# Optimization experiments

Measured on AMD Instinct MI355X. Metric: run time of the kernel, lower is better.

## Reference

```python
import jax, jax.numpy as jnp
import numpy as np

EPS = 1e-5


def _in_relu(y):
    # instance norm (no affine, biased var, eps=1e-5) + ReLU, y: [B,C,H,W]
    mu = jnp.mean(y, axis=(-2, -1), keepdims=True)
    var = jnp.mean((y - mu) ** 2, axis=(-2, -1), keepdims=True)
    return jax.nn.relu((y - mu) * jax.lax.rsqrt(var + EPS))


def _conv3(x, w, b):
    # x: [C,H,W], w: [O,I,3,3] -> [O,H,W]
    y = jax.lax.conv_general_dilated(x[None], w, (1, 1), ((1, 1), (1, 1)),
                                     dimension_numbers=('NCHW', 'OIHW', 'NCHW'))[0]
    return y + b[:, None, None]


def _mod_block(x, W, b, mod):
    # per-sample weight modulation: mod[n] * W, then conv+IN+relu; x: [B,C,H,W], mod: [B,O,I,3,3]
    y = jax.vmap(lambda xi, mi: _conv3(xi, mi * W, b))(x, mod)
    return _in_relu(y)


def _maxpool2(x):
    return jax.lax.reduce_window(x, -jnp.inf, jax.lax.max, (1, 1, 2, 2), (1, 1, 2, 2), 'VALID')


def _up2(x):
    B, C, H, W = x.shape
    # bilinear, half-pixel centers == PyTorch align_corners=False
    return jax.image.resize(x, (B, C, 2 * H, 2 * W), method='bilinear')


def _conv1x1(x, w, b):
    y = jax.lax.conv_general_dilated(x, w, (1, 1), 'VALID',
                                     dimension_numbers=('NCHW', 'OIHW', 'NCHW'))
    return y + b[None, :, None, None]


def setup_inputs() -> dict:
    key = jax.random.key(0)
    B, H, W = 8, 256, 256
    ks = iter(jax.random.split(key, 64))
    d = {}
    d['us_query_input'] = jax.random.normal(next(ks), (B, 1, H, W), jnp.float32)
    d['ksp_query_imgs'] = jax.random.normal(next(ks), (B, H, W, 2), jnp.float32)
    d['ksp_mask_query'] = jax.random.uniform(next(ks), (B, H, W), jnp.float32)
    down_io = [(1, 32), (32, 64), (64, 128), (128, 256)]
    up_io = [(512, 128), (256, 64), (128, 32), (64, 32)]
    for i, (ci, co) in enumerate(down_io):
        d[f'down_mod_{i}'] = jax.random.normal(next(ks), (B, co, ci, 3, 3), jnp.float32)
        d[f'W_d{i}'] = 0.05 * jax.random.normal(next(ks), (co, ci, 3, 3), jnp.float32)
        d[f'b_d{i}'] = 0.05 * jax.random.normal(next(ks), (co,), jnp.float32)
    d['latent_mod'] = jax.random.normal(next(ks), (B, 256, 256, 3, 3), jnp.float32)
    d['W_lat'] = 0.05 * jax.random.normal(next(ks), (256, 256, 3, 3), jnp.float32)
    d['b_lat'] = 0.05 * jax.random.normal(next(ks), (256,), jnp.float32)
    for i, (ci, co) in enumerate(up_io):
        d[f'up_mod_{i}'] = jax.random.normal(next(ks), (B, co, ci, 3, 3), jnp.float32)
        d[f'W_u{i}'] = 0.05 * jax.random.normal(next(ks), (co, ci, 3, 3), jnp.float32)
        d[f'b_u{i}'] = 0.05 * jax.random.normal(next(ks), (co,), jnp.float32)
    d['w_c1'] = 0.05 * jax.random.normal(next(ks), (16, 32, 1, 1), jnp.float32)
    d['b_c1'] = 0.05 * jax.random.normal(next(ks), (16,), jnp.float32)
    d['w_c2'] = 0.05 * jax.random.normal(next(ks), (1, 16, 1, 1), jnp.float32)
    d['b_c2'] = 0.05 * jax.random.normal(next(ks), (1,), jnp.float32)
    d['w_c3'] = 0.05 * jax.random.normal(next(ks), (1, 1, 1, 1), jnp.float32)
    d['b_c3'] = 0.05 * jax.random.normal(next(ks), (1,), jnp.float32)
    return d


def reference(us_query_input, ksp_query_imgs, ksp_mask_query,
              down_mod_0, down_mod_1, down_mod_2, down_mod_3,
              latent_mod, up_mod_0, up_mod_1, up_mod_2, up_mod_3,
              W_d0, b_d0, W_d1, b_d1, W_d2, b_d2, W_d3, b_d3,
              W_lat, b_lat,
              W_u0, b_u0, W_u1, b_u1, W_u2, b_u2, W_u3, b_u3,
              w_c1, b_c1, w_c2, b_c2, w_c3, b_c3):
    x0 = us_query_input
    out = x0
    skips = []
    downs = [(W_d0, b_d0, down_mod_0), (W_d1, b_d1, down_mod_1),
             (W_d2, b_d2, down_mod_2), (W_d3, b_d3, down_mod_3)]
    for Wc, bc, m in downs:
        out = _mod_block(out, Wc, bc, m)
        skips.append(out)
        out = _maxpool2(out)
    out = _mod_block(out, W_lat, b_lat, latent_mod)
    ups = [(W_u0, b_u0, up_mod_0), (W_u1, b_u1, up_mod_1),
           (W_u2, b_u2, up_mod_2), (W_u3, b_u3, up_mod_3)]
    for Wc, bc, m in ups:
        out = _up2(out)
        out = jnp.concatenate([out, skips.pop()], axis=1)
        out = _mod_block(out, Wc, bc, m)
    out = _conv1x1(_conv1x1(_conv1x1(out, w_c1, b_c1), w_c2, b_c2), w_c3, b_c3)
    out = out + x0
    # FFT data consistency
    pred = out[:, 0]                                  # [B,H,W]
    kpred = jnp.fft.fft2(pred, norm='ortho')
    ksp = ksp_query_imgs[..., 0] + 1j * ksp_query_imgs[..., 1]
    upd = ksp_mask_query * ksp + (1.0 - ksp_mask_query) * kpred
    img = jnp.fft.ifft2(upd, norm='ortho')
    return jnp.real(img)[:, None].astype(jnp.float32)   # [B,1,H,W]
```

## Files before the change

kernel.cpp:

```cpp
#include <hip/hip_runtime.h>


#define EPS_IN 1e-5f

typedef __attribute__((ext_vector_type(8))) short short8;
typedef __attribute__((ext_vector_type(4))) short short4_t;
typedef __attribute__((ext_vector_type(4))) float f32x4;

__device__ __forceinline__ short f2bf(float f) {
    unsigned u = __float_as_uint(f);
    unsigned r = (u + 0x7fffu + ((u >> 16) & 1u)) >> 16;
    return (short)r;
}
__device__ __forceinline__ float bf2f(short s) {
    return __uint_as_float(((unsigned)(unsigned short)s) << 16);
}

__global__ void zero_f(float* __restrict__ p, int n)
{
    int i = blockIdx.x * 256 + threadIdx.x;
    if (i < n) p[i] = 0.f;
}

__global__ void make_wm(const float* __restrict__ W, const float* __restrict__ mod,
                        short* __restrict__ wm, int Co, int Ci)
{
    int idx = blockIdx.x * 256 + threadIdx.x;
    int total = 8 * Co * Ci;
    if (idx >= total) return;
    int ci = idx % Ci;
    int rem = idx / Ci;
    int co = rem % Co;
    int b = rem / Co;
    const float* wp = W + (size_t)(co * Ci + ci) * 9;
    const float* mp = mod + ((size_t)((size_t)b * Co + co) * Ci + ci) * 9;
#pragma unroll
    for (int k = 0; k < 9; ++k)
        wm[(((size_t)(b * 9 + k) * Co + co) * Ci + ci)] = f2bf(wp[k] * mp[k]);
}

template <int VR, int NCOG>
__global__ __launch_bounds__(256) void conv3x3_cl(
    const short* __restrict__ x1, int Ci1,
    const short* __restrict__ x2,
    const short* __restrict__ wm,
    short* __restrict__ y,
    float2* __restrict__ stats,
    int Ci, int Co, int H, int W)
{
    constexpr int TH = 4 * VR, SH = TH + 2, SW = 18;
    __shared__ short s_x[SH][SW][32];
    __shared__ float s_red[4][4][NCOG][4][2];

    const int tid = threadIdx.x;
    const int lane = tid & 63, wv = tid >> 6;
    const int m = lane & 15, g = lane >> 4;
    const int tilesx = W >> 4;
    const int tx0 = (blockIdx.x % tilesx) * 16;
    const int ty0 = (blockIdx.x / tilesx) * TH;
    const int co0 = blockIdx.y * (16 * NCOG);
    const int b = blockIdx.z;
    const int Ci2 = Ci - Ci1;

    f32x4 acc[NCOG][VR];
#pragma unroll
    for (int cg = 0; cg < NCOG; ++cg)
#pragma unroll
        for (int r = 0; r < VR; ++r) acc[cg][r] = (f32x4)0.f;

    const short* wmb = wm + (size_t)b * 9 * Co * Ci;

    for (int ci0 = 0; ci0 < Ci; ci0 += 32) {
        const short* src; int C, cb;
        if (ci0 < Ci1) { src = x1 + (size_t)b * H * W * Ci1; C = Ci1; cb = ci0; }
        else           { src = x2 + (size_t)b * H * W * Ci2; C = Ci2; cb = ci0 - Ci1; }
        __syncthreads();
        for (int idx = tid; idx < SH * SW * 4; idx += 256) {
            int gg = idx & 3, pos = idx >> 2;
            int yy = pos / SW, xx = pos - yy * SW;
            int gy = ty0 + yy - 1, gx = tx0 + xx - 1;
            short8 v = (short8)0;
            if (gy >= 0 && gy < H && gx >= 0 && gx < W)
                v = *(const short8*)(src + ((size_t)gy * W + gx) * C + cb + gg * 8);
            *(short8*)&s_x[yy][xx][(gg ^ (xx & 3)) * 8] = v;
        }
        __syncthreads();
#pragma unroll
        for (int t = 0; t < 9; ++t) {
            const int dy = t / 3, dx = t - 3 * (t / 3);
            const short* wr = wmb + ((size_t)t * Co + co0) * Ci + ci0 + g * 8;
            short8 a[NCOG];
#pragma unroll
            for (int cg = 0; cg < NCOG; ++cg)
                a[cg] = *(const short8*)(wr + (size_t)(cg * 16 + m) * Ci);
            const int xx = m + dx;
            const int sgo = (g ^ (xx & 3)) * 8;
#pragma unroll
            for (int r = 0; r < VR; ++r) {
                short8 bf = *(const short8*)&s_x[wv * VR + r + dy][xx][sgo];
#pragma unroll
                for (int cg = 0; cg < NCOG; ++cg)
                    acc[cg][r] = __builtin_amdgcn_mfma_f32_16x16x32_bf16(a[cg], bf, acc[cg][r], 0, 0, 0);
            }
        }
    }

    const int ox = tx0 + m;
#pragma unroll
    for (int cg = 0; cg < NCOG; ++cg)
#pragma unroll
        for (int r = 0; r < VR; ++r) {
            int oy = ty0 + wv * VR + r;
            short4_t o;
#pragma unroll
            for (int q = 0; q < 4; ++q) o[q] = f2bf(acc[cg][r][q]);
            *(short4_t*)(y + (((size_t)b * H + oy) * W + ox) * Co + co0 + cg * 16 + g * 4) = o;
        }

#pragma unroll
    for (int cg = 0; cg < NCOG; ++cg)
#pragma unroll
        for (int q = 0; q < 4; ++q) {
            float s = 0.f, s2 = 0.f;
#pragma unroll
            for (int r = 0; r < VR; ++r) { float v = acc[cg][r][q]; s += v; s2 += v * v; }
#pragma unroll
            for (int msk = 1; msk < 16; msk <<= 1) { s += __shfl_xor(s, msk); s2 += __shfl_xor(s2, msk); }
            if (m == 0) { s_red[wv][g][cg][q][0] = s; s_red[wv][g][cg][q][1] = s2; }
        }
    __syncthreads();
    for (int i = tid; i < 16 * NCOG; i += 256) {
        int q = i & 3, gg = (i >> 2) & 3, cg = i >> 4;
        float S = 0.f, S2 = 0.f;
#pragma unroll
        for (int w = 0; w < 4; ++w) { S += s_red[w][gg][cg][q][0]; S2 += s_red[w][gg][cg][q][1]; }
        float* sp = (float*)&stats[(size_t)b * Co + co0 + i];
        atomicAdd(sp, S); atomicAdd(sp + 1, S2);
    }
}

__global__ __launch_bounds__(256) void conv_d0_cl(
    const float* __restrict__ x0, const float* __restrict__ W,
    const float* __restrict__ mod, short* __restrict__ y,
    float2* __restrict__ stats)
{
    __shared__ float s[18][18];
    __shared__ float sw[32][9];
    __shared__ float s_red[4][32][2];
    const int tid = threadIdx.x;
    const int tx = tid & 15, ty = tid >> 4;
    const int tx0 = (blockIdx.x & 15) * 16, ty0 = (blockIdx.x >> 4) * 16;
    const int b = blockIdx.y;
    if (tid < 288) sw[tid / 9][tid % 9] = W[tid] * mod[b * 288 + tid];
    for (int pos = tid; pos < 18 * 18; pos += 256) {
        int yy = pos / 18, xx = pos - yy * 18;
        int gy = ty0 + yy - 1, gx = tx0 + xx - 1;
        bool inb = gy >= 0 && gy < 256 && gx >= 0 && gx < 256;
        s[yy][xx] = inb ? x0[((size_t)b << 16) + gy * 256 + gx] : 0.f;
    }
    __syncthreads();
    float v[3][3];
#pragma unroll
    for (int r = 0; r < 3; ++r)
#pragma unroll
        for (int c = 0; c < 3; ++c) v[r][c] = s[ty + r][tx + c];
    float vals[32];
#pragma unroll
    for (int co = 0; co < 32; ++co) {
        float a = 0.f;
#pragma unroll
        for (int r = 0; r < 3; ++r)
#pragma unroll
            for (int c = 0; c < 3; ++c) a = fmaf(v[r][c], sw[co][r * 3 + c], a);
        vals[co] = a;
    }
    short* yp = y + (((size_t)b * 256 + ty0 + ty) * 256 + tx0 + tx) * 32;
#pragma unroll
    for (int j = 0; j < 4; ++j) {
        short8 o;
#pragma unroll
        for (int e = 0; e < 8; ++e) o[e] = f2bf(vals[j * 8 + e]);
        *(short8*)(yp + j * 8) = o;
    }
    const int lane = tid & 63, wv = tid >> 6;
#pragma unroll
    for (int co = 0; co < 32; ++co) {
        float sm = vals[co], s2 = vals[co] * vals[co];
#pragma unroll
        for (int off = 32; off > 0; off >>= 1) { sm += __shfl_down(sm, off); s2 += __shfl_down(s2, off); }
        if (lane == 0) { s_red[wv][co][0] = sm; s_red[wv][co][1] = s2; }
    }
    __syncthreads();
    if (tid < 32) {
        float S = 0.f, S2 = 0.f;
#pragma unroll
        for (int w = 0; w < 4; ++w) { S += s_red[w][tid][0]; S2 += s_red[w][tid][1]; }
        float* sp = (float*)&stats[(size_t)b * 32 + tid];
        atomicAdd(sp, S); atomicAdd(sp + 1, S2);
    }
}

__global__ __launch_bounds__(256) void norm_relu_cl(
    short* __restrict__ y, const float2* __restrict__ stats,
    int Co, int n8 , float invHW)
{
    __shared__ float2 st[256];
    const int b = blockIdx.y;
    for (int i = threadIdx.x; i < Co; i += 256) {
        float2 v = stats[(size_t)b * Co + i];
        float mu = v.x * invHW;
        float var = v.y * invHW - mu * mu;
        st[i] = make_float2(mu, rsqrtf(var + EPS_IN));
    }
    __syncthreads();
    const int c8m = (Co >> 3) - 1;
    short8* base = (short8*)(y + (size_t)b * n8 * 8);
    for (int i = blockIdx.x * 256 + threadIdx.x; i < n8; i += gridDim.x * 256) {
        int c0 = (i & c8m) * 8;
        short8 v = base[i];
#pragma unroll
        for (int e = 0; e < 8; ++e) {
            float2 s = st[c0 + e];
            v[e] = f2bf(fmaxf(0.f, (bf2f(v[e]) - s.x) * s.y));
        }
        base[i] = v;
    }
}

__global__ void maxpool_cl(const short* __restrict__ in, short* __restrict__ out,
                           int c8s, int ws, int hs, int total8)
{
    const int C = 8 << c8s;
    for (int idx = blockIdx.x * 256 + threadIdx.x; idx < total8; idx += gridDim.x * 256) {
        int c8 = idx & ((1 << c8s) - 1);
        int p = idx >> c8s;
        int x = p & ((1 << ws) - 1);
        int yy = (p >> ws) & ((1 << hs) - 1);
        int b = p >> (ws + hs);
        const short* ip = in + (((size_t)b * (2 << hs) + 2 * yy) * (2 << ws) + 2 * x) * C + c8 * 8;
        size_t rs = (size_t)(2 << ws) * C;
        short8 v0 = *(const short8*)ip, v1 = *(const short8*)(ip + C);
        short8 v2 = *(const short8*)(ip + rs), v3 = *(const short8*)(ip + rs + C);
        short8 o;
#pragma unroll
        for (int e = 0; e < 8; ++e)
            o[e] = f2bf(fmaxf(fmaxf(bf2f(v0[e]), bf2f(v1[e])), fmaxf(bf2f(v2[e]), bf2f(v3[e]))));
        *(short8*)(out + (size_t)idx * 8) = o;
    }
}

__global__ void upsample_cl(const short* __restrict__ in, short* __restrict__ out,
                            int c8s, int wsi, int hsi, int total8)
{
    const int C = 8 << c8s;
    const int Win = 1 << wsi, Hin = 1 << hsi;
    for (int idx = blockIdx.x * 256 + threadIdx.x; idx < total8; idx += gridDim.x * 256) {
        int c8 = idx & ((1 << c8s) - 1);
        int p = idx >> c8s;
        int x = p & (2 * Win - 1);
        int yy = (p >> (wsi + 1)) & (2 * Hin - 1);
        int b = p >> (wsi + 1 + hsi + 1);
        int xk = x >> 1, yk = yy >> 1;
        int xa, xb; float wxa;
        if (x & 1) { xa = xk; xb = (xk + 1 < Win) ? xk + 1 : Win - 1; wxa = 0.75f; }
        else       { xa = (xk > 0) ? xk - 1 : 0; xb = xk; wxa = 0.25f; }
        int ya, yb; float wya;
        if (yy & 1) { ya = yk; yb = (yk + 1 < Hin) ? yk + 1 : Hin - 1; wya = 0.75f; }
        else        { ya = (yk > 0) ? yk - 1 : 0; yb = yk; wya = 0.25f; }
        const short* ib = in + (size_t)b * Hin * Win * C + c8 * 8;
        short8 vaa = *(const short8*)(ib + ((size_t)ya * Win + xa) * C);
        short8 vab = *(const short8*)(ib + ((size_t)ya * Win + xb) * C);
        short8 vba = *(const short8*)(ib + ((size_t)yb * Win + xa) * C);
        short8 vbb = *(const short8*)(ib + ((size_t)yb * Win + xb) * C);
        short8 o;
#pragma unroll
        for (int e = 0; e < 8; ++e) {
            float r0 = wxa * bf2f(vaa[e]) + (1.f - wxa) * bf2f(vab[e]);
            float r1 = wxa * bf2f(vba[e]) + (1.f - wxa) * bf2f(vbb[e]);
            o[e] = f2bf(wya * r0 + (1.f - wya) * r1);
        }
        *(short8*)(out + (size_t)idx * 8) = o;
    }
}

__global__ void eff1x1(const float* __restrict__ w1, const float* __restrict__ b1,
                       const float* __restrict__ w2, const float* __restrict__ b2,
                       const float* __restrict__ w3, const float* __restrict__ b3,
                       float* __restrict__ eff)
{
    int t = threadIdx.x;
    if (t < 32) {
        float s = 0.f;
        for (int k = 0; k < 16; ++k) s += w2[k] * w1[k * 32 + t];
        eff[t] = w3[0] * s;
    }
    if (t == 32) {
        float s = 0.f;
        for (int k = 0; k < 16; ++k) s += w2[k] * b1[k];
        eff[32] = w3[0] * (s + b2[0]) + b3[0];
    }
}

__global__ void final_pred_cl(const short* __restrict__ act, const float* __restrict__ x0,
                              const float* __restrict__ eff, float* __restrict__ pred)
{
    int idx = blockIdx.x * 256 + threadIdx.x;
    const short8* a = (const short8*)(act + (size_t)idx * 32);
    float s = eff[32] + x0[idx];
#pragma unroll
    for (int j = 0; j < 4; ++j) {
        short8 v = a[j];
#pragma unroll
        for (int e = 0; e < 8; ++e) s += eff[j * 8 + e] * bf2f(v[e]);
    }
    pred[idx] = s;
}

__device__ __forceinline__ void fft256(float2* s, int tid, float sign)
{
    __syncthreads();
#pragma unroll
    for (int t = 0; t < 4; ++t) {
        int i = tid + t * 64;
        int r = __brev(i) >> 24;
        if (r > i) { float2 tmp = s[i]; s[i] = s[r]; s[r] = tmp; }
    }
    __syncthreads();
    for (int st = 1; st <= 8; ++st) {
        int m = 1 << st, half = m >> 1;
#pragma unroll
        for (int t = 0; t < 2; ++t) {
            int k = tid + t * 64;
            int g = k >> (st - 1), j = k & (half - 1);
            int i0 = (g << st) + j, i1 = i0 + half;
            float ang = sign * 6.283185307179586f * (float)j / (float)m;
            float sn, cs;
            __sincosf(ang, &sn, &cs);
            float2 a = s[i0], b = s[i1];
            float2 tt = make_float2(b.x * cs - b.y * sn, b.x * sn + b.y * cs);
            s[i0] = make_float2(a.x + tt.x, a.y + tt.y);
            s[i1] = make_float2(a.x - tt.x, a.y - tt.y);
        }
        __syncthreads();
    }
}

__global__ __launch_bounds__(64) void fft_rows_fwd(const float* __restrict__ pred,
                                                   float2* __restrict__ out)
{
    __shared__ float2 s[256];
    int row = blockIdx.x, tid = threadIdx.x;
    const float* p = pred + (size_t)row * 256;
    for (int i = tid; i < 256; i += 64) s[i] = make_float2(p[i], 0.f);
    fft256(s, tid, -1.f);
    float2* o = out + (size_t)row * 256;
    for (int i = tid; i < 256; i += 64) o[i] = s[i];
}

__global__ __launch_bounds__(64) void fft_cols_combine(float2* __restrict__ data,
                                                       const float* __restrict__ ksp,
                                                       const float* __restrict__ mask)
{
    __shared__ float2 s[256];
    int col = blockIdx.x & 255, b = blockIdx.x >> 8;
    int tid = threadIdx.x;
    float2* base = data + (size_t)b * 65536 + col;
    for (int i = tid; i < 256; i += 64) s[i] = base[(size_t)i * 256];
    fft256(s, tid, -1.f);
    for (int i = tid; i < 256; i += 64) {
        size_t mi = ((size_t)b * 256 + i) * 256 + col;
        float m = mask[mi];
        float2 kp = s[i];
        float kr = ksp[mi * 2], ki = ksp[mi * 2 + 1];
        s[i] = make_float2(m * kr + (1.f - m) * kp.x * (1.f / 256.f),
                           m * ki + (1.f - m) * kp.y * (1.f / 256.f));
    }
    fft256(s, tid, 1.f);
    for (int i = tid; i < 256; i += 64) base[(size_t)i * 256] = s[i];
}

__global__ __launch_bounds__(64) void fft_rows_inv(const float2* __restrict__ data,
                                                   float* __restrict__ out)
{
    __shared__ float2 s[256];
    int row = blockIdx.x, tid = threadIdx.x;
    const float2* p = data + (size_t)row * 256;
    for (int i = tid; i < 256; i += 64) s[i] = p[i];
    fft256(s, tid, 1.f);
    float* o = out + (size_t)row * 256;
    for (int i = tid; i < 256; i += 64) o[i] = s[i].x * (1.f / 256.f);
}

extern "C" void kernel_launch(void* const* d_in, const int* in_sizes, int n_in,
                              void* d_out, int out_size, void* d_ws, size_t ws_size,
                              hipStream_t stream)
{
    (void)in_sizes; (void)n_in; (void)out_size; (void)ws_size;

    const float* x0 = (const float*)d_in[0];
    const float* ksp = (const float*)d_in[1];
    const float* mask = (const float*)d_in[2];
    const float* mod_d[4] = {(const float*)d_in[3], (const float*)d_in[6],
                             (const float*)d_in[9], (const float*)d_in[12]};
    const float* W_d[4] = {(const float*)d_in[4], (const float*)d_in[7],
                           (const float*)d_in[10], (const float*)d_in[13]};
    const float* mod_lat = (const float*)d_in[15];
    const float* W_lat = (const float*)d_in[16];
    const float* mod_u[4] = {(const float*)d_in[18], (const float*)d_in[21],
                             (const float*)d_in[24], (const float*)d_in[27]};
    const float* W_u[4] = {(const float*)d_in[19], (const float*)d_in[22],
                           (const float*)d_in[25], (const float*)d_in[28]};
    const float* w_c1 = (const float*)d_in[30];
    const float* b_c1 = (const float*)d_in[31];
    const float* w_c2 = (const float*)d_in[32];
    const float* b_c2 = (const float*)d_in[33];
    const float* w_c3 = (const float*)d_in[34];
    const float* b_c3 = (const float*)d_in[35];

    short* sA  = (short*)d_ws;
    short* sB  = sA + 16777216;
    short* sk0 = sB + 16777216;
    short* sk1 = sk0 + 16777216;
    short* sk2 = sk1 + 8388608;
    short* sk3 = sk2 + 4194304;
    short* wm  = sk3 + 2097152;
    float* pred = (float*)(wm + 4718592);
    float2* cplx = (float2*)(pred + 524288);
    float2* stA = cplx + 524288;
    float* eff = (float*)(stA + 7936);

    float2* st_d0 = stA + 0;
    float2* st_d1 = stA + 256;
    float2* st_d2 = stA + 768;
    float2* st_d3 = stA + 1792;
    float2* st_lat = stA + 3840;
    float2* st_u0 = stA + 5888;
    float2* st_u1 = stA + 6912;
    float2* st_u2 = stA + 7424;
    float2* st_u3 = stA + 7680;

    dim3 blk(256);

    zero_f<<<62, blk, 0, stream>>>((float*)stA, 15872);
    eff1x1<<<1, 64, 0, stream>>>(w_c1, b_c1, w_c2, b_c2, w_c3, b_c3, eff);

    conv_d0_cl<<<dim3(256, 8), blk, 0, stream>>>(x0, W_d[0], mod_d[0], sk0, st_d0);
    norm_relu_cl<<<dim3(512, 8), blk, 0, stream>>>(sk0, st_d0, 32, 262144, 1.f / 65536.f);
    maxpool_cl<<<2048, blk, 0, stream>>>(sk0, sA, 2, 7, 7, 524288);

    make_wm<<<(8 * 64 * 32 + 255) / 256, blk, 0, stream>>>(W_d[1], mod_d[1], wm, 64, 32);
    conv3x3_cl<4, 4><<<dim3(64, 1, 8), blk, 0, stream>>>(sA, 32, sA, wm, sk1, st_d1, 32, 64, 128, 128);
    norm_relu_cl<<<dim3(256, 8), blk, 0, stream>>>(sk1, st_d1, 64, 131072, 1.f / 16384.f);
    maxpool_cl<<<1024, blk, 0, stream>>>(sk1, sA, 3, 6, 6, 262144);

    make_wm<<<(8 * 128 * 64 + 255) / 256, blk, 0, stream>>>(W_d[2], mod_d[2], wm, 128, 64);
    conv3x3_cl<2, 4><<<dim3(32, 2, 8), blk, 0, stream>>>(sA, 64, sA, wm, sk2, st_d2, 64, 128, 64, 64);
    norm_relu_cl<<<dim3(128, 8), blk, 0, stream>>>(sk2, st_d2, 128, 65536, 1.f / 4096.f);
    maxpool_cl<<<512, blk, 0, stream>>>(sk2, sA, 4, 5, 5, 131072);

    make_wm<<<(8 * 256 * 128 + 255) / 256, blk, 0, stream>>>(W_d[3], mod_d[3], wm, 256, 128);
    conv3x3_cl<2, 2><<<dim3(8, 8, 8), blk, 0, stream>>>(sA, 128, sA, wm, sk3, st_d3, 128, 256, 32, 32);
    norm_relu_cl<<<dim3(64, 8), blk, 0, stream>>>(sk3, st_d3, 256, 32768, 1.f / 1024.f);
    maxpool_cl<<<256, blk, 0, stream>>>(sk3, sA, 5, 4, 4, 65536);

    make_wm<<<(8 * 256 * 256 + 255) / 256, blk, 0, stream>>>(W_lat, mod_lat, wm, 256, 256);
    conv3x3_cl<2, 1><<<dim3(2, 16, 8), blk, 0, stream>>>(sA, 256, sA, wm, sB, st_lat, 256, 256, 16, 16);
    norm_relu_cl<<<dim3(32, 8), blk, 0, stream>>>(sB, st_lat, 256, 8192, 1.f / 256.f);

    upsample_cl<<<1024, blk, 0, stream>>>(sB, sA, 5, 4, 4, 262144);
    make_wm<<<(8 * 128 * 512 + 255) / 256, blk, 0, stream>>>(W_u[0], mod_u[0], wm, 128, 512);
    conv3x3_cl<2, 1><<<dim3(8, 8, 8), blk, 0, stream>>>(sA, 256, sk3, wm, sB, st_u0, 512, 128, 32, 32);
    norm_relu_cl<<<dim3(32, 8), blk, 0, stream>>>(sB, st_u0, 128, 16384, 1.f / 1024.f);

    upsample_cl<<<2048, blk, 0, stream>>>(sB, sA, 4, 5, 5, 524288);
    make_wm<<<(8 * 64 * 256 + 255) / 256, blk, 0, stream>>>(W_u[1], mod_u[1], wm, 64, 256);
    conv3x3_cl<2, 2><<<dim3(32, 2, 8), blk, 0, stream>>>(sA, 128, sk2, wm, sB, st_u1, 256, 64, 64, 64);
    norm_relu_cl<<<dim3(64, 8), blk, 0, stream>>>(sB, st_u1, 64, 32768, 1.f / 4096.f);

    upsample_cl<<<4096, blk, 0, stream>>>(sB, sA, 3, 6, 6, 1048576);
    make_wm<<<(8 * 32 * 128 + 255) / 256, blk, 0, stream>>>(W_u[2], mod_u[2], wm, 32, 128);
    conv3x3_cl<4, 2><<<dim3(64, 1, 8), blk, 0, stream>>>(sA, 64, sk1, wm, sB, st_u2, 128, 32, 128, 128);
    norm_relu_cl<<<dim3(128, 8), blk, 0, stream>>>(sB, st_u2, 32, 65536, 1.f / 16384.f);

    upsample_cl<<<8192, blk, 0, stream>>>(sB, sA, 2, 7, 7, 2097152);
    make_wm<<<(8 * 32 * 64 + 255) / 256, blk, 0, stream>>>(W_u[3], mod_u[3], wm, 32, 64);
    conv3x3_cl<4, 2><<<dim3(256, 1, 8), blk, 0, stream>>>(sA, 32, sk0, wm, sB, st_u3, 64, 32, 256, 256);
    norm_relu_cl<<<dim3(512, 8), blk, 0, stream>>>(sB, st_u3, 32, 262144, 1.f / 65536.f);

    final_pred_cl<<<2048, blk, 0, stream>>>(sB, x0, eff, pred);

    fft_rows_fwd<<<2048, 64, 0, stream>>>(pred, cplx);
    fft_cols_combine<<<2048, 64, 0, stream>>>(cplx, ksp, mask);
    fft_rows_inv<<<2048, 64, 0, stream>>>(cplx, (float*)d_out);
}
```

Measured before the change: 543.8 us.

## Fuse instance-norm+ReLU into consumers and register-prefetch conv input chunks

Removes the standalone norm_relu pass over every conv output. Normalization and ReLU are now applied lazily where the data is consumed: in maxpool, bilinear upsample, the skip-connection half of the next conv's shared-memory staging, and the final 1x1 prediction. The conv kernel also prefetches the next 32-channel input chunk into registers while computing the current one. This saves a full read and write of each activation tensor, at the cost of recomputing rsqrt per element in the pool and upsample kernels and extra register pressure in the conv.

```diff
diff --git a/kernel.cpp b/kernel.cpp
--- a/kernel.cpp
+++ b/kernel.cpp
@@ -43,14 +43,17 @@
 __global__ __launch_bounds__(256) void conv3x3_cl(
     const short* __restrict__ x1, int Ci1,
     const short* __restrict__ x2,
+    const float2* __restrict__ st2, float invHW2,
     const short* __restrict__ wm,
     short* __restrict__ y,
     float2* __restrict__ stats,
     int Ci, int Co, int H, int W)
 {
     constexpr int TH = 4 * VR, SH = TH + 2, SW = 18;
+    constexpr int NST = (SH * SW * 4 + 255) / 256;
     __shared__ short s_x[SH][SW][32];
     __shared__ float s_red[4][4][NCOG][4][2];
+    __shared__ float2 s_st[256];
 
     const int tid = threadIdx.x;
     const int lane = tid & 63, wv = tid >> 6;
@@ -62,6 +65,13 @@
     const int b = blockIdx.z;
     const int Ci2 = Ci - Ci1;
 
+    for (int i = tid; i < Ci2; i += 256) {
+        float2 v = st2[(size_t)b * Ci2 + i];
+        float mu = v.x * invHW2;
+        float var = v.y * invHW2 - mu * mu;
+        s_st[i] = make_float2(mu, rsqrtf(var + EPS_IN));
+    }
+
     f32x4 acc[NCOG][VR];
 #pragma unroll
     for (int cg = 0; cg < NCOG; ++cg)
@@ -70,21 +80,55 @@
 
     const short* wmb = wm + (size_t)b * 9 * Co * Ci;
 
-    for (int ci0 = 0; ci0 < Ci; ci0 += 32) {
+    short8 stg[NST];
+    auto load_chunk = [&](int ci0) {
         const short* src; int C, cb;
         if (ci0 < Ci1) { src = x1 + (size_t)b * H * W * Ci1; C = Ci1; cb = ci0; }
         else           { src = x2 + (size_t)b * H * W * Ci2; C = Ci2; cb = ci0 - Ci1; }
+#pragma unroll
+        for (int it = 0; it < NST; ++it) {
+            int idx = tid + it * 256;
+            short8 v = (short8)0;
+            if (idx < SH * SW * 4) {
+                int gg = idx & 3, pos = idx >> 2;
+                int yy = pos / SW, xx = pos - yy * SW;
+                int gy = ty0 + yy - 1, gx = tx0 + xx - 1;
+                if (gy >= 0 && gy < H && gx >= 0 && gx < W)
+                    v = *(const short8*)(src + ((size_t)gy * W + gx) * C + cb + gg * 8);
+            }
+            stg[it] = v;
+        }
+    };
+
+    load_chunk(0);
+
+    for (int ci0 = 0; ci0 < Ci; ci0 += 32) {
         __syncthreads();
-        for (int idx = tid; idx < SH * SW * 4; idx += 256) {
-            int gg = idx & 3, pos = idx >> 2;
-            int yy = pos / SW, xx = pos - yy * SW;
-            int gy = ty0 + yy - 1, gx = tx0 + xx - 1;
-            short8 v = (short8)0;
-            if (gy >= 0 && gy < H && gx >= 0 && gx < W)
-                v = *(const short8*)(src + ((size_t)gy * W + gx) * C + cb + gg * 8);
-            *(short8*)&s_x[yy][xx][(gg ^ (xx & 3)) * 8] = v;
+        const bool nrm = (ci0 >= Ci1);
+        const int cb = nrm ? (ci0 - Ci1) : ci0;
+#pragma unroll
+        for (int it = 0; it < NST; ++it) {
+            int idx = tid + it * 256;
+            if (idx < SH * SW * 4) {
+                int gg = idx & 3, pos = idx >> 2;
+                int yy = pos / SW, xx = pos - yy * SW;
+                short8 v = stg[it];
+                if (nrm) {
+                    int gy = ty0 + yy - 1, gx = tx0 + xx - 1;
+                    if (gy >= 0 && gy < H && gx >= 0 && gx < W) {
+#pragma unroll
+                        for (int e = 0; e < 8; ++e) {
+                            float2 s = s_st[cb + gg * 8 + e];
+                            v[e] = f2bf(fmaxf(0.f, (bf2f(v[e]) - s.x) * s.y));
+                        }
+                    }
+                }
+                *(short8*)&s_x[yy][xx][(gg ^ (xx & 3)) * 8] = v;
+            }
         }
         __syncthreads();
+        if (ci0 + 32 < Ci) load_chunk(ci0 + 32);
+
 #pragma unroll
         for (int t = 0; t < 9; ++t) {
             const int dy = t / 3, dx = t - 3 * (t / 3);
@@ -200,34 +244,9 @@
     }
 }
 
-__global__ __launch_bounds__(256) void norm_relu_cl(
-    short* __restrict__ y, const float2* __restrict__ stats,
-    int Co, int n8 , float invHW)
-{
-    __shared__ float2 st[256];
-    const int b = blockIdx.y;
-    for (int i = threadIdx.x; i < Co; i += 256) {
-        float2 v = stats[(size_t)b * Co + i];
-        float mu = v.x * invHW;
-        float var = v.y * invHW - mu * mu;
-        st[i] = make_float2(mu, rsqrtf(var + EPS_IN));
-    }
-    __syncthreads();
-    const int c8m = (Co >> 3) - 1;
-    short8* base = (short8*)(y + (size_t)b * n8 * 8);
-    for (int i = blockIdx.x * 256 + threadIdx.x; i < n8; i += gridDim.x * 256) {
-        int c0 = (i & c8m) * 8;
-        short8 v = base[i];
-#pragma unroll
-        for (int e = 0; e < 8; ++e) {
-            float2 s = st[c0 + e];
-            v[e] = f2bf(fmaxf(0.f, (bf2f(v[e]) - s.x) * s.y));
-        }
-        base[i] = v;
-    }
-}
-
-__global__ void maxpool_cl(const short* __restrict__ in, short* __restrict__ out,
+__global__ void maxpool_cl(const short* __restrict__ in,
+                           const float2* __restrict__ st, float invHW,
+                           short* __restrict__ out,
                            int c8s, int ws, int hs, int total8)
 {
     const int C = 8 << c8s;
@@ -243,13 +262,20 @@
         short8 v2 = *(const short8*)(ip + rs), v3 = *(const short8*)(ip + rs + C);
         short8 o;
 #pragma unroll
-        for (int e = 0; e < 8; ++e)
-            o[e] = f2bf(fmaxf(fmaxf(bf2f(v0[e]), bf2f(v1[e])), fmaxf(bf2f(v2[e]), bf2f(v3[e]))));
+        for (int e = 0; e < 8; ++e) {
+            float mx = fmaxf(fmaxf(bf2f(v0[e]), bf2f(v1[e])), fmaxf(bf2f(v2[e]), bf2f(v3[e])));
+            float2 sv = st[(size_t)b * C + c8 * 8 + e];
+            float mu = sv.x * invHW;
+            float rsig = rsqrtf(sv.y * invHW - mu * mu + EPS_IN);
+            o[e] = f2bf(fmaxf(0.f, (mx - mu) * rsig));
+        }
         *(short8*)(out + (size_t)idx * 8) = o;
     }
 }
 
-__global__ void upsample_cl(const short* __restrict__ in, short* __restrict__ out,
+__global__ void upsample_cl(const short* __restrict__ in,
+                            const float2* __restrict__ st, float invHW,
+                            short* __restrict__ out,
                             int c8s, int wsi, int hsi, int total8)
 {
     const int C = 8 << c8s;
@@ -275,8 +301,15 @@
         short8 o;
 #pragma unroll
         for (int e = 0; e < 8; ++e) {
-            float r0 = wxa * bf2f(vaa[e]) + (1.f - wxa) * bf2f(vab[e]);
-            float r1 = wxa * bf2f(vba[e]) + (1.f - wxa) * bf2f(vbb[e]);
+            float2 sv = st[(size_t)b * C + c8 * 8 + e];
+            float mu = sv.x * invHW;
+            float rsig = rsqrtf(sv.y * invHW - mu * mu + EPS_IN);
+            float aa = fmaxf(0.f, (bf2f(vaa[e]) - mu) * rsig);
+            float ab = fmaxf(0.f, (bf2f(vab[e]) - mu) * rsig);
+            float ba = fmaxf(0.f, (bf2f(vba[e]) - mu) * rsig);
+            float bb = fmaxf(0.f, (bf2f(vbb[e]) - mu) * rsig);
+            float r0 = wxa * aa + (1.f - wxa) * ab;
+            float r1 = wxa * ba + (1.f - wxa) * bb;
             o[e] = f2bf(wya * r0 + (1.f - wya) * r1);
         }
         *(short8*)(out + (size_t)idx * 8) = o;
@@ -301,17 +334,31 @@
     }
 }
 
-__global__ void final_pred_cl(const short* __restrict__ act, const float* __restrict__ x0,
-                              const float* __restrict__ eff, float* __restrict__ pred)
-{
+__global__ __launch_bounds__(256) void final_pred_cl(
+    const short* __restrict__ act, const float2* __restrict__ st, float invHW,
+    const float* __restrict__ x0, const float* __restrict__ eff,
+    float* __restrict__ pred)
+{
+    __shared__ float2 s_st[32];
     int idx = blockIdx.x * 256 + threadIdx.x;
+    int b = idx >> 16;
+    if (threadIdx.x < 32) {
+        float2 v = st[(size_t)b * 32 + threadIdx.x];
+        float mu = v.x * invHW;
+        s_st[threadIdx.x] = make_float2(mu, rsqrtf(v.y * invHW - mu * mu + EPS_IN));
+    }
+    __syncthreads();
     const short8* a = (const short8*)(act + (size_t)idx * 32);
     float s = eff[32] + x0[idx];
 #pragma unroll
     for (int j = 0; j < 4; ++j) {
         short8 v = a[j];
 #pragma unroll
-        for (int e = 0; e < 8; ++e) s += eff[j * 8 + e] * bf2f(v[e]);
+        for (int e = 0; e < 8; ++e) {
+            float2 sv = s_st[j * 8 + e];
+            float f = fmaxf(0.f, (bf2f(v[e]) - sv.x) * sv.y);
+            s += eff[j * 8 + e] * f;
+        }
     }
     pred[idx] = s;
 }
@@ -439,55 +486,49 @@
     float2* st_u2 = stA + 7424;
     float2* st_u3 = stA + 7680;
 
+    const float i64k = 1.f / 65536.f, i16k = 1.f / 16384.f, i4k = 1.f / 4096.f,
+                i1k = 1.f / 1024.f, i256 = 1.f / 256.f;
+
     dim3 blk(256);
 
     zero_f<<<62, blk, 0, stream>>>((float*)stA, 15872);
     eff1x1<<<1, 64, 0, stream>>>(w_c1, b_c1, w_c2, b_c2, w_c3, b_c3, eff);
 
     conv_d0_cl<<<dim3(256, 8), blk, 0, stream>>>(x0, W_d[0], mod_d[0], sk0, st_d0);
-    norm_relu_cl<<<dim3(512, 8), blk, 0, stream>>>(sk0, st_d0, 32, 262144, 1.f / 65536.f);
-    maxpool_cl<<<2048, blk, 0, stream>>>(sk0, sA, 2, 7, 7, 524288);
+    maxpool_cl<<<2048, blk, 0, stream>>>(sk0, st_d0, i64k, sA, 2, 7, 7, 524288);
 
     make_wm<<<(8 * 64 * 32 + 255) / 256, blk, 0, stream>>>(W_d[1], mod_d[1], wm, 64, 32);
-    conv3x3_cl<4, 4><<<dim3(64, 1, 8), blk, 0, stream>>>(sA, 32, sA, wm, sk1, st_d1, 32, 64, 128, 128);
-    norm_relu_cl<<<dim3(256, 8), blk, 0, stream>>>(sk1, st_d1, 64, 131072, 1.f / 16384.f);
-    maxpool_cl<<<1024, blk, 0, stream>>>(sk1, sA, 3, 6, 6, 262144);
+    conv3x3_cl<4, 4><<<dim3(64, 1, 8), blk, 0, stream>>>(sA, 32, sA, stA, 0.f, wm, sk1, st_d1, 32, 64, 128, 128);
+    maxpool_cl<<<1024, blk, 0, stream>>>(sk1, st_d1, i16k, sA, 3, 6, 6, 262144);
 
     make_wm<<<(8 * 128 * 64 + 255) / 256, blk, 0, stream>>>(W_d[2], mod_d[2], wm, 128, 64);
-    conv3x3_cl<2, 4><<<dim3(32, 2, 8), blk, 0, stream>>>(sA, 64, sA, wm, sk2, st_d2, 64, 128, 64, 64);
-    norm_relu_cl<<<dim3(128, 8), blk, 0, stream>>>(sk2, st_d2, 128, 65536, 1.f / 4096.f);
-    maxpool_cl<<<512, blk, 0, stream>>>(sk2, sA, 4, 5, 5, 131072);
+    conv3x3_cl<2, 4><<<dim3(32, 2, 8), blk, 0, stream>>>(sA, 64, sA, stA, 0.f, wm, sk2, st_d2, 64, 128, 64, 64);
+    maxpool_cl<<<512, blk, 0, stream>>>(sk2, st_d2, i4k, sA, 4, 5, 5, 131072);
 
     make_wm<<<(8 * 256 * 128 + 255) / 256, blk, 0, stream>>>(W_d[3], mod_d[3], wm, 256, 128);
-    conv3x3_cl<2, 2><<<dim3(8, 8, 8), blk, 0, stream>>>(sA, 128, sA, wm, sk3, st_d3, 128, 256, 32, 32);
-    norm_relu_cl<<<dim3(64, 8), blk, 0, stream>>>(sk3, st_d3, 256, 32768, 1.f / 1024.f);
-    maxpool_cl<<<256, blk, 0, stream>>>(sk3, sA, 5, 4, 4, 65536);
+    conv3x3_cl<2, 2><<<dim3(8, 8, 8), blk, 0, stream>>>(sA, 128, sA, stA, 0.f, wm, sk3, st_d3, 128, 256, 32, 32);
+    maxpool_cl<<<256, blk, 0, stream>>>(sk3, st_d3, i1k, sA, 5, 4, 4, 65536);
 
     make_wm<<<(8 * 256 * 256 + 255) / 256, blk, 0, stream>>>(W_lat, mod_lat, wm, 256, 256);
-    conv3x3_cl<2, 1><<<dim3(2, 16, 8), blk, 0, stream>>>(sA, 256, sA, wm, sB, st_lat, 256, 256, 16, 16);
-    norm_relu_cl<<<dim3(32, 8), blk, 0, stream>>>(sB, st_lat, 256, 8192, 1.f / 256.f);
-
-    upsample_cl<<<1024, blk, 0, stream>>>(sB, sA, 5, 4, 4, 262144);
+    conv3x3_cl<2, 1><<<dim3(2, 16, 8), blk, 0, stream>>>(sA, 256, sA, stA, 0.f, wm, sB, st_lat, 256, 256, 16, 16);
+
+    upsample_cl<<<1024, blk, 0, stream>>>(sB, st_lat, i256, sA, 5, 4, 4, 262144);
     make_wm<<<(8 * 128 * 512 + 255) / 256, blk, 0, stream>>>(W_u[0], mod_u[0], wm, 128, 512);
-    conv3x3_cl<2, 1><<<dim3(8, 8, 8), blk, 0, stream>>>(sA, 256, sk3, wm, sB, st_u0, 512, 128, 32, 32);
-    norm_relu_cl<<<dim3(32, 8), blk, 0, stream>>>(sB, st_u0, 128, 16384, 1.f / 1024.f);
-
-    upsample_cl<<<2048, blk, 0, stream>>>(sB, sA, 4, 5, 5, 524288);
+    conv3x3_cl<2, 1><<<dim3(8, 8, 8), blk, 0, stream>>>(sA, 256, sk3, st_d3, i1k, wm, sB, st_u0, 512, 128, 32, 32);
+
+    upsample_cl<<<2048, blk, 0, stream>>>(sB, st_u0, i1k, sA, 4, 5, 5, 524288);
     make_wm<<<(8 * 64 * 256 + 255) / 256, blk, 0, stream>>>(W_u[1], mod_u[1], wm, 64, 256);
-    conv3x3_cl<2, 2><<<dim3(32, 2, 8), blk, 0, stream>>>(sA, 128, sk2, wm, sB, st_u1, 256, 64, 64, 64);
-    norm_relu_cl<<<dim3(64, 8), blk, 0, stream>>>(sB, st_u1, 64, 32768, 1.f / 4096.f);
-
-    upsample_cl<<<4096, blk, 0, stream>>>(sB, sA, 3, 6, 6, 1048576);
+    conv3x3_cl<2, 2><<<dim3(32, 2, 8), blk, 0, stream>>>(sA, 128, sk2, st_d2, i4k, wm, sB, st_u1, 256, 64, 64, 64);
+
+    upsample_cl<<<4096, blk, 0, stream>>>(sB, st_u1, i4k, sA, 3, 6, 6, 1048576);
     make_wm<<<(8 * 32 * 128 + 255) / 256, blk, 0, stream>>>(W_u[2], mod_u[2], wm, 32, 128);
-    conv3x3_cl<4, 2><<<dim3(64, 1, 8), blk, 0, stream>>>(sA, 64, sk1, wm, sB, st_u2, 128, 32, 128, 128);
-    norm_relu_cl<<<dim3(128, 8), blk, 0, stream>>>(sB, st_u2, 32, 65536, 1.f / 16384.f);
-
-    upsample_cl<<<8192, blk, 0, stream>>>(sB, sA, 2, 7, 7, 2097152);
+    conv3x3_cl<4, 2><<<dim3(64, 1, 8), blk, 0, stream>>>(sA, 64, sk1, st_d1, i16k, wm, sB, st_u2, 128, 32, 128, 128);
+
+    upsample_cl<<<8192, blk, 0, stream>>>(sB, st_u2, i16k, sA, 2, 7, 7, 2097152);
     make_wm<<<(8 * 32 * 64 + 255) / 256, blk, 0, stream>>>(W_u[3], mod_u[3], wm, 32, 64);
-    conv3x3_cl<4, 2><<<dim3(256, 1, 8), blk, 0, stream>>>(sA, 32, sk0, wm, sB, st_u3, 64, 32, 256, 256);
-    norm_relu_cl<<<dim3(512, 8), blk, 0, stream>>>(sB, st_u3, 32, 262144, 1.f / 65536.f);
-
-    final_pred_cl<<<2048, blk, 0, stream>>>(sB, x0, eff, pred);
+    conv3x3_cl<4, 2><<<dim3(256, 1, 8), blk, 0, stream>>>(sA, 32, sk0, st_d0, i64k, wm, sB, st_u3, 64, 32, 256, 256);
+
+    final_pred_cl<<<2048, blk, 0, stream>>>(sB, st_u3, i64k, x0, eff, pred);
 
     fft_rows_fwd<<<2048, 64, 0, stream>>>(pred, cplx);
     fft_cols_combine<<<2048, 64, 0, stream>>>(cplx, ksp, mask);
```

Measured after the change: 562.4 us. +3.4%, slower.
